# Optimization experiments

Hardware: AMD Instinct MI355X
Metric: run time of the kernel (lower is better)

## Reference

```python
import jax, jax.numpy as jnp
import numpy as np

N_EMBD = 1024
HEAD_SIZE = 64
B, T = 8, 2048


def setup_inputs() -> dict:
    key = jax.random.key(0)
    kx, kq, kk, kv = jax.random.split(key, 4)
    s = 1.0 / np.sqrt(N_EMBD)  # ~ torch Linear init scale
    return {
        "x": jax.random.normal(kx, (B, T, N_EMBD), dtype=jnp.float32),
        "Wq": jax.random.normal(kq, (N_EMBD, HEAD_SIZE), dtype=jnp.float32) * s,
        "Wk": jax.random.normal(kk, (N_EMBD, HEAD_SIZE), dtype=jnp.float32) * s,
        "Wv": jax.random.normal(kv, (N_EMBD, HEAD_SIZE), dtype=jnp.float32) * s,
    }


def reference(x, Wq, Wk, Wv):
    # x: [B,T,C]; single-head causal self-attention (dropout p=0.0 / eval)
    q = jnp.einsum("btc,cd->btd", x, Wq)
    k = jnp.einsum("btc,cd->btd", x, Wk)
    v = jnp.einsum("btc,cd->btd", x, Wv)
    scale = 1.0 / np.sqrt(HEAD_SIZE).astype(np.float32)
    scores = jnp.einsum("bqd,bkd->bqk", q, k) * scale  # [B,T,T]
    Tq = x.shape[1]
    causal = jnp.tril(jnp.ones((Tq, Tq), dtype=bool))
    scores = jnp.where(causal[None, :, :], scores, -jnp.inf)
    attn = jax.nn.softmax(scores, axis=-1)
    out = jnp.einsum("bqk,bkd->bqd", attn, v)  # [B,T,head_size]
    return out
```

## Files before the change

### kernel.cpp

```cpp
#include <hip/hip_runtime.h>
#include <hip/hip_bf16.h>

#define BATCH 8
#define SEQ   2048
#define CDIM  1024
#define HDIM  64
#define NROWS (BATCH*SEQ)
#define NSPLIT 8

typedef __attribute__((ext_vector_type(8))) short bf16x8;
typedef __attribute__((ext_vector_type(4))) float f32x4;

#define QSCALE 0.18033688011112042f
#define SFIX 24.0f

__device__ inline ushort f2bf(float f) {
    union { float f; uint u; } x; x.f = f;
    uint r = (x.u + 0x7fffu + ((x.u >> 16) & 1u)) >> 16;
    return (ushort)r;
}

__global__ __launch_bounds__(256) void wpack_kernel(
    const float* __restrict__ Wq, const float* __restrict__ Wk,
    const float* __restrict__ Wv, ushort* __restrict__ wp2)
{
    const int g = blockIdx.x * 256 + threadIdx.x;
    const int l15  = g & 15;
    const int hi   = (g >> 4) & 3;
    const int c32  = (g >> 6) & 1;
    const int step = (g >> 7) & 15;
    const int f    = g >> 11;
    const int n = f * 16 + l15;
    const int which = n >> 6, nl = n & 63;
    const float* W = (which == 0) ? Wq : (which == 1) ? Wk : Wv;
    const float sc = (which == 0) ? QSCALE : 1.0f;
    const int c0 = step * 64 + c32 * 32 + hi * 8;

    ushort v[8];
    #pragma unroll
    for (int j = 0; j < 8; ++j)
        v[j] = f2bf(W[(size_t)(c0 + j) * HDIM + nl] * sc);
    uint4 pack;
    pack.x = (uint)v[0] | ((uint)v[1] << 16);
    pack.y = (uint)v[2] | ((uint)v[3] << 16);
    pack.z = (uint)v[4] | ((uint)v[5] << 16);
    pack.w = (uint)v[6] | ((uint)v[7] << 16);
    reinterpret_cast<uint4*>(wp2)[g] = pack;
}

__global__ __launch_bounds__(512, 4) void qkv_gemm(
    const float* __restrict__ x, const ushort* __restrict__ wp2,
    ushort* __restrict__ qb, ushort* __restrict__ kbuf, ushort* __restrict__ vt)
{
    __shared__ ushort xs[2][32 * 64];
    const int t = threadIdx.x;
    const int w = t >> 6, lane = t & 63;
    const int l15 = lane & 15, hi = lane >> 4;
    const int rowg = w & 1, colg = w >> 1;
    const int m0 = blockIdx.x * 32;

    f32x4 acc[3];
    #pragma unroll
    for (int i = 0; i < 3; ++i) acc[i] = (f32x4){0.f, 0.f, 0.f, 0.f};

    const int xrow = t >> 4, xc4 = t & 15;
    float4 xra, xrb;
    const ushort* wbase = wp2 + (size_t)lane * 8;

#define LOADX(S, KK)                                                           \
    xr##S = reinterpret_cast<const float4*>(x + (size_t)(m0 + xrow) * CDIM + (KK))[xc4];

#define WRITEX(S, BUF)                                                         \
    {                                                                          \
        ushort4 bx = make_ushort4(f2bf(xr##S.x), f2bf(xr##S.y), f2bf(xr##S.z), f2bf(xr##S.w)); \
        int xb = (xrow * 128 + xc4 * 8) ^ ((xrow & 7) << 4);                   \
        *reinterpret_cast<ushort4*>(reinterpret_cast<char*>(xs[BUF]) + xb) = bx; \
    }

#define MFMA_STEP(BUF, STEP)                                                   \
    {                                                                          \
        const int arow = rowg * 16 + l15;                                      \
        bf16x8 bf[6];                                                          \
        _Pragma("unroll")                                                      \
        for (int nf = 0; nf < 3; ++nf) {                                       \
            const int f = colg * 3 + nf;                                       \
            bf[nf * 2 + 0] = *reinterpret_cast<const bf16x8*>(wbase + (size_t)(f * 16 + (STEP)) * 1024);       \
            bf[nf * 2 + 1] = *reinterpret_cast<const bf16x8*>(wbase + (size_t)(f * 16 + (STEP)) * 1024 + 512); \
        }                                                                      \
        _Pragma("unroll")                                                      \
        for (int c32 = 0; c32 < 2; ++c32) {                                    \
            const int abyte = (arow * 128 + hi * 16 + c32 * 64) ^ ((arow & 7) << 4); \
            bf16x8 a = *reinterpret_cast<const bf16x8*>(reinterpret_cast<char*>(xs[BUF]) + abyte); \
            _Pragma("unroll")                                                  \
            for (int nf = 0; nf < 3; ++nf)                                     \
                acc[nf] = __builtin_amdgcn_mfma_f32_16x16x32_bf16(a, bf[nf * 2 + c32], acc[nf], 0, 0, 0); \
        }                                                                      \
    }

    LOADX(a, 0)
    LOADX(b, 64)
    WRITEX(a, 0)
    __syncthreads();

    for (int step = 0; step < 16; step += 2) {
        if (step + 2 < 16) { LOADX(a, (step + 2) * 64) }
        MFMA_STEP(0, step)
        WRITEX(b, 1)
        __syncthreads();
        if (step + 3 < 16) { LOADX(b, (step + 3) * 64) }
        MFMA_STEP(1, step + 1)
        if (step + 2 < 16) { WRITEX(a, 0) }
        __syncthreads();
    }
#undef LOADX
#undef WRITEX
#undef MFMA_STEP

    #pragma unroll
    for (int nf = 0; nf < 3; ++nf) {
        const int n = colg * 48 + nf * 16 + l15;
        #pragma unroll
        for (int r = 0; r < 4; ++r) {
            const int grow = m0 + rowg * 16 + hi * 4 + r;
            const ushort bv = f2bf(acc[nf][r]);
            if (n < 64) {
                qb[(size_t)grow * 64 + n] = bv;
            } else if (n < 128) {
                kbuf[(size_t)grow * 64 + (n - 64)] = bv;
            } else {
                const int b = grow >> 11, tt = grow & 2047;
                vt[(((size_t)b * 64 + (n - 128)) << 11) + tt] = bv;
            }
        }
    }
}

__global__ __launch_bounds__(256, 4) void attn_flash(
    const ushort* __restrict__ qb, const ushort* __restrict__ kbuf,
    const ushort* __restrict__ vt, ushort* __restrict__ Opart,
    float* __restrict__ lpart)
{
    __shared__ ushort kst[2][64 * 64];
    __shared__ ushort vst[2][64 * 64];
    __shared__ ushort P[4][1024];

    const int t = threadIdx.x;
    const int w = t >> 6, lane = t & 63;
    const int l15 = lane & 15, hi = lane >> 4;
    const int bid = blockIdx.x;
    const int pid = (bid & 7) * 128 + (bid >> 3);
    const int batch = pid >> 7;
    const int rem = pid & 127;
    const int pairIdx = rem >> 3;
    const int s = rem & 7;
    const int qtA = pairIdx, qtB = 31 - pairIdx;
    const int ntA = qtA + 1;

    const ushort* kB = kbuf + (size_t)batch * SEQ * 64;
    const ushort* vB = vt + (size_t)batch * 64 * SEQ;
    ushort* Osp = Opart + (size_t)s * NROWS * 64;
    float* lsp = lpart + (size_t)s * NROWS;
    char* pw = reinterpret_cast<char*>(P[w]);

    const int r0 = t >> 3, c8 = t & 7;
    const int r1 = r0 + 32;
    const int sb0 = (r0 * 128 + c8 * 16) ^ ((r0 & 7) << 4);
    const int sb1 = (r1 * 128 + c8 * 16) ^ ((r1 & 7) << 4);

    uint4 kr0, kr1, vr0, vr1;

#define STAGE_ISSUE(C)                                                        \
    {                                                                         \
        const int kt_ = ((C) >= ntA) ? ((C) - ntA) : (C);                     \
        const int j0_ = kt_ * 64;                                             \
        kr0 = *reinterpret_cast<const uint4*>(kB + (size_t)(j0_ + r0) * 64 + c8 * 8); \
        kr1 = *reinterpret_cast<const uint4*>(kB + (size_t)(j0_ + r1) * 64 + c8 * 8); \
        vr0 = *reinterpret_cast<const uint4*>(vB + (size_t)r0 * SEQ + j0_ + c8 * 8);  \
        vr1 = *reinterpret_cast<const uint4*>(vB + (size_t)r1 * SEQ + j0_ + c8 * 8);  \
    }

#define STAGE_WRITE(BUF)                                                      \
    {                                                                         \
        *reinterpret_cast<uint4*>(reinterpret_cast<char*>(kst[BUF]) + sb0) = kr0; \
        *reinterpret_cast<uint4*>(reinterpret_cast<char*>(kst[BUF]) + sb1) = kr1; \
        *reinterpret_cast<uint4*>(reinterpret_cast<char*>(vst[BUF]) + sb0) = vr0; \
        *reinterpret_cast<uint4*>(reinterpret_cast<char*>(vst[BUF]) + sb1) = vr1; \
    }

#define LOADQ(QT)                                                             \
    {                                                                         \
        const ushort* qp_ = qb + (size_t)(batch * SEQ + (QT) * 64 + w * 16 + l15) * 64 + hi * 8; \
        aq0 = *reinterpret_cast<const bf16x8*>(qp_);                          \
        aq1 = *reinterpret_cast<const bf16x8*>(qp_ + 32);                     \
    }

#define DUMP(QT)                                                              \
    {                                                                         \
        _Pragma("unroll")                                                     \
        for (int dt = 0; dt < 4; ++dt)                                        \
            _Pragma("unroll")                                                 \
            for (int r = 0; r < 4; ++r)                                       \
                Osp[(size_t)(batch * SEQ + (QT) * 64 + w * 16 + hi * 4 + r) * 64 + dt * 16 + l15] = f2bf(O[dt][r]); \
        _Pragma("unroll")                                                     \
        for (int r = 0; r < 4; ++r) {                                         \
            float s_ = lsum[r];                                               \
            s_ += __shfl_xor(s_, 1, 64);                                      \
            s_ += __shfl_xor(s_, 2, 64);                                      \
            s_ += __shfl_xor(s_, 4, 64);                                      \
            s_ += __shfl_xor(s_, 8, 64);                                      \
            if (l15 == 0)                                                     \
                lsp[batch * SEQ + (QT) * 64 + w * 16 + hi * 4 + r] = s_;      \
        }                                                                     \
    }

#define RESET_STATE()                                                         \
    {                                                                         \
        _Pragma("unroll")                                                     \
        for (int i = 0; i < 4; ++i) {                                         \
            O[i] = (f32x4){0.f, 0.f, 0.f, 0.f};                               \
            lsum[i] = 0.f;                                                    \
        }                                                                     \
    }

    bf16x8 aq0, aq1;
    LOADQ(qtA)
    f32x4 O[4];
    float lsum[4];
    RESET_STATE()

    STAGE_ISSUE(s)
    STAGE_WRITE(0)
    __syncthreads();

    int curB = 0, cur = 0;
    for (int c = s; c < 33; c += 8) {
        if (c + 8 < 33) { STAGE_ISSUE(c + 8) }
        if (c >= ntA && !curB) {
            DUMP(qtA)
            RESET_STATE()
            LOADQ(qtB)
            curB = 1;
        }
        const int qt = curB ? qtB : qtA;
        const int kt = curB ? (c - ntA) : c;
        const int j0 = kt * 64;
        const int qrow0 = qt * 64 + w * 16;
        const bool diag = curB ? (c == 32) : (c == ntA - 1);

        const char* kc = reinterpret_cast<const char*>(kst[cur]);
        const char* vc = reinterpret_cast<const char*>(vst[cur]);

        f32x4 S[4];
        #pragma unroll
        for (int kb = 0; kb < 4; ++kb) {
            const int key = kb * 16 + l15;
            const int sw = (key & 7) << 4;
            bf16x8 b0 = *reinterpret_cast<const bf16x8*>(kc + ((key * 128 + hi * 16) ^ sw));
            bf16x8 b1 = *reinterpret_cast<const bf16x8*>(kc + ((key * 128 + hi * 16 + 64) ^ sw));
            f32x4 z = (f32x4){0.f, 0.f, 0.f, 0.f};
            z = __builtin_amdgcn_mfma_f32_16x16x32_bf16(aq0, b0, z, 0, 0, 0);
            z = __builtin_amdgcn_mfma_f32_16x16x32_bf16(aq1, b1, z, 0, 0, 0);
            S[kb] = z;
        }
        if (diag) {
            #pragma unroll
            for (int kb = 0; kb < 4; ++kb) {
                const int key = j0 + kb * 16 + l15;
                #pragma unroll
                for (int r = 0; r < 4; ++r) {
                    const int qr = qrow0 + hi * 4 + r;
                    if (key > qr) S[kb][r] = -1e30f;
                }
            }
        }
        #pragma unroll
        for (int kb = 0; kb < 4; ++kb)
            #pragma unroll
            for (int r = 0; r < 4; ++r)
                S[kb][r] = exp2f(S[kb][r] - SFIX);
        #pragma unroll
        for (int r = 0; r < 4; ++r)
            lsum[r] += (S[0][r] + S[1][r]) + (S[2][r] + S[3][r]);

        #pragma unroll
        for (int kb = 0; kb < 4; ++kb) {
            #pragma unroll
            for (int r = 0; r < 4; ++r) {
                const int prow = hi * 4 + r;
                const int pcol = kb * 16 + l15;
                const int byte = (prow * 128 + pcol * 2) ^ ((prow & 7) << 4);
                *reinterpret_cast<ushort*>(pw + byte) = f2bf(S[kb][r]);
            }
        }
        asm volatile("" ::: "memory");
        const int pb0 = (l15 * 128 + hi * 16) ^ ((l15 & 7) << 4);
        const int pb1 = (l15 * 128 + hi * 16 + 64) ^ ((l15 & 7) << 4);
        bf16x8 pa0 = *reinterpret_cast<const bf16x8*>(pw + pb0);
        bf16x8 pa1 = *reinterpret_cast<const bf16x8*>(pw + pb1);
        #pragma unroll
        for (int dt = 0; dt < 4; ++dt) {
            const int d = dt * 16 + l15;
            const int sw = (d & 7) << 4;
            bf16x8 v0 = *reinterpret_cast<const bf16x8*>(vc + ((d * 128 + hi * 16) ^ sw));
            bf16x8 v1 = *reinterpret_cast<const bf16x8*>(vc + ((d * 128 + hi * 16 + 64) ^ sw));
            O[dt] = __builtin_amdgcn_mfma_f32_16x16x32_bf16(pa0, v0, O[dt], 0, 0, 0);
            O[dt] = __builtin_amdgcn_mfma_f32_16x16x32_bf16(pa1, v1, O[dt], 0, 0, 0);
        }
        if (c + 8 < 33) { STAGE_WRITE(cur ^ 1) }
        __syncthreads();
        cur ^= 1;
    }

    DUMP(qtB)
#undef STAGE_ISSUE
#undef STAGE_WRITE
#undef LOADQ
#undef DUMP
#undef RESET_STATE
}

__global__ __launch_bounds__(256) void merge_kernel(
    const ushort* __restrict__ Opart, const float* __restrict__ lpart,
    float* __restrict__ out)
{
    const int idx = blockIdx.x * 256 + threadIdx.x;
    const int row = idx >> 3;
    float acc[8] = {0.f, 0.f, 0.f, 0.f, 0.f, 0.f, 0.f, 0.f};
    float lv = 0.f;
    #pragma unroll
    for (int s = 0; s < NSPLIT; ++s) {
        uint4 v = reinterpret_cast<const uint4*>(Opart + (size_t)s * NROWS * 64)[idx];
        const uint u0 = v.x, u1 = v.y, u2 = v.z, u3 = v.w;
        acc[0] += __uint_as_float((u0 & 0xffffu) << 16);
        acc[1] += __uint_as_float(u0 & 0xffff0000u);
        acc[2] += __uint_as_float((u1 & 0xffffu) << 16);
        acc[3] += __uint_as_float(u1 & 0xffff0000u);
        acc[4] += __uint_as_float((u2 & 0xffffu) << 16);
        acc[5] += __uint_as_float(u2 & 0xffff0000u);
        acc[6] += __uint_as_float((u3 & 0xffffu) << 16);
        acc[7] += __uint_as_float(u3 & 0xffff0000u);
        lv += lpart[s * NROWS + row];
    }
    const float inv = 1.0f / lv;
    float4 o0 = make_float4(acc[0] * inv, acc[1] * inv, acc[2] * inv, acc[3] * inv);
    float4 o1 = make_float4(acc[4] * inv, acc[5] * inv, acc[6] * inv, acc[7] * inv);
    reinterpret_cast<float4*>(out)[idx * 2]     = o0;
    reinterpret_cast<float4*>(out)[idx * 2 + 1] = o1;
}

extern "C" void kernel_launch(void* const* d_in, const int* in_sizes, int n_in,
                              void* d_out, int out_size, void* d_ws, size_t ws_size,
                              hipStream_t stream) {
    const float* x  = (const float*)d_in[0];
    const float* Wq = (const float*)d_in[1];
    const float* Wk = (const float*)d_in[2];
    const float* Wv = (const float*)d_in[3];
    float* out = (float*)d_out;

    ushort* qb   = (ushort*)d_ws;
    ushort* kbuf = qb + (size_t)NROWS * 64;
    ushort* vt   = kbuf + (size_t)NROWS * 64;
    ushort* wp2  = vt + (size_t)NROWS * 64;
    float* lpart = (float*)(wp2 + 192 * 1024);
    ushort* Opart = (ushort*)(lpart + (size_t)NSPLIT * NROWS);

    wpack_kernel<<<96, 256, 0, stream>>>(Wq, Wk, Wv, wp2);
    qkv_gemm<<<NROWS / 32, 512, 0, stream>>>(x, wp2, qb, kbuf, vt);
    attn_flash<<<1024, 256, 0, stream>>>(qb, kbuf, vt, Opart, lpart);
    merge_kernel<<<(NROWS * HDIM / 8) / 256, 256, 0, stream>>>(Opart, lpart, out);
}
```

Baseline: 53.40 us.

## Stage packed QKV weights into LDS with async direct global-to-LDS loads

The weight pack is changed to a swizzled per-step layout, and the QKV GEMM now copies each 64-wide K-step of the weights into a double-buffered LDS tile with global_load_lds. It then reads the B fragments from LDS instead of having every wave fetch them from global memory. This removes the duplicated global/L2 weight traffic across the row groups and lets the weight loads overlap with the MFMA work. In exchange it adds 48KB of LDS per block, which likely cuts the number of resident blocks per CU below the launch-bounds target. Correctness also relies on the barriers waiting for the async LDS loads to finish.

Result: no change. 52.44 us (-1.8%).

```diff
diff --git a/kernel.cpp b/kernel.cpp
--- a/kernel.cpp
+++ b/kernel.cpp
@@ -20,39 +20,45 @@
     return (ushort)r;
 }
 
+__device__ inline void gload_lds16(const void* gsrc, void* ldst) {
+    __builtin_amdgcn_global_load_lds(
+        (const __attribute__((address_space(1))) unsigned int*)gsrc,
+        (__attribute__((address_space(3))) unsigned int*)ldst,
+        16, 0, 0);
+}
+
 __global__ __launch_bounds__(256) void wpack_kernel(
     const float* __restrict__ Wq, const float* __restrict__ Wk,
-    const float* __restrict__ Wv, ushort* __restrict__ wp2)
+    const float* __restrict__ Wv, ushort* __restrict__ wp3)
 {
     const int g = blockIdx.x * 256 + threadIdx.x;
-    const int l15  = g & 15;
-    const int hi   = (g >> 4) & 3;
-    const int c32  = (g >> 6) & 1;
-    const int step = (g >> 7) & 15;
-    const int f    = g >> 11;
-    const int n = f * 16 + l15;
+    const int s = g / 1536;
+    const int i = g % 1536;
+    const int n = i >> 3;
+    const int b0 = ((i & 7) * 16) ^ ((n & 7) << 4);
+    const int c0 = s * 64 + (b0 >> 1);
     const int which = n >> 6, nl = n & 63;
     const float* W = (which == 0) ? Wq : (which == 1) ? Wk : Wv;
     const float sc = (which == 0) ? QSCALE : 1.0f;
-    const int c0 = step * 64 + c32 * 32 + hi * 8;
 
     ushort v[8];
     #pragma unroll
-    for (int j = 0; j < 8; ++j)
-        v[j] = f2bf(W[(size_t)(c0 + j) * HDIM + nl] * sc);
+    for (int k = 0; k < 8; ++k)
+        v[k] = f2bf(W[(size_t)(c0 + k) * HDIM + nl] * sc);
     uint4 pack;
     pack.x = (uint)v[0] | ((uint)v[1] << 16);
     pack.y = (uint)v[2] | ((uint)v[3] << 16);
     pack.z = (uint)v[4] | ((uint)v[5] << 16);
     pack.w = (uint)v[6] | ((uint)v[7] << 16);
-    reinterpret_cast<uint4*>(wp2)[g] = pack;
+    reinterpret_cast<uint4*>(wp3)[g] = pack;
 }
 
 __global__ __launch_bounds__(512, 4) void qkv_gemm(
-    const float* __restrict__ x, const ushort* __restrict__ wp2,
+    const float* __restrict__ x, const ushort* __restrict__ wp3,
     ushort* __restrict__ qb, ushort* __restrict__ kbuf, ushort* __restrict__ vt)
 {
     __shared__ ushort xs[2][32 * 64];
+    __shared__ ushort ws[2][192 * 64];
     const int t = threadIdx.x;
     const int w = t >> 6, lane = t & 63;
     const int l15 = lane & 15, hi = lane >> 4;
@@ -65,7 +71,16 @@
 
     const int xrow = t >> 4, xc4 = t & 15;
     float4 xra, xrb;
-    const ushort* wbase = wp2 + (size_t)lane * 8;
+
+#define GLOADW(STEP, BUF)                                                      \
+    {                                                                          \
+        _Pragma("unroll")                                                      \
+        for (int j = 0; j < 3; ++j) {                                          \
+            const int chunk = j * 512 + w * 64;                                \
+            gload_lds16(wp3 + ((size_t)(STEP) * 1536 + chunk + lane) * 8,      \
+                        reinterpret_cast<char*>(ws[BUF]) + chunk * 16);        \
+        }                                                                      \
+    }
 
 #define LOADX(S, KK)                                                           \
     xr##S = reinterpret_cast<const float4*>(x + (size_t)(m0 + xrow) * CDIM + (KK))[xc4];
@@ -77,26 +92,25 @@
         *reinterpret_cast<ushort4*>(reinterpret_cast<char*>(xs[BUF]) + xb) = bx; \
     }
 
-#define MFMA_STEP(BUF, STEP)                                                   \
+#define MFMA_STEP(BUF)                                                         \
     {                                                                          \
         const int arow = rowg * 16 + l15;                                      \
-        bf16x8 bf[6];                                                          \
-        _Pragma("unroll")                                                      \
-        for (int nf = 0; nf < 3; ++nf) {                                       \
-            const int f = colg * 3 + nf;                                       \
-            bf[nf * 2 + 0] = *reinterpret_cast<const bf16x8*>(wbase + (size_t)(f * 16 + (STEP)) * 1024);       \
-            bf[nf * 2 + 1] = *reinterpret_cast<const bf16x8*>(wbase + (size_t)(f * 16 + (STEP)) * 1024 + 512); \
-        }                                                                      \
         _Pragma("unroll")                                                      \
         for (int c32 = 0; c32 < 2; ++c32) {                                    \
             const int abyte = (arow * 128 + hi * 16 + c32 * 64) ^ ((arow & 7) << 4); \
             bf16x8 a = *reinterpret_cast<const bf16x8*>(reinterpret_cast<char*>(xs[BUF]) + abyte); \
             _Pragma("unroll")                                                  \
-            for (int nf = 0; nf < 3; ++nf)                                     \
-                acc[nf] = __builtin_amdgcn_mfma_f32_16x16x32_bf16(a, bf[nf * 2 + c32], acc[nf], 0, 0, 0); \
+            for (int nf = 0; nf < 3; ++nf) {                                   \
+                const int n = colg * 48 + nf * 16 + l15;                       \
+                const int bbyte = (n * 128 + hi * 16 + c32 * 64) ^ ((n & 7) << 4); \
+                bf16x8 b = *reinterpret_cast<const bf16x8*>(reinterpret_cast<char*>(ws[BUF]) + bbyte); \
+                acc[nf] = __builtin_amdgcn_mfma_f32_16x16x32_bf16(a, b, acc[nf], 0, 0, 0); \
+            }                                                                  \
         }                                                                      \
     }
 
+    GLOADW(0, 0)
+    GLOADW(1, 1)
     LOADX(a, 0)
     LOADX(b, 64)
     WRITEX(a, 0)
@@ -104,14 +118,17 @@
 
     for (int step = 0; step < 16; step += 2) {
         if (step + 2 < 16) { LOADX(a, (step + 2) * 64) }
-        MFMA_STEP(0, step)
+        MFMA_STEP(0)
         WRITEX(b, 1)
         __syncthreads();
+        if (step + 2 < 16) { GLOADW(step + 2, 0) }
         if (step + 3 < 16) { LOADX(b, (step + 3) * 64) }
-        MFMA_STEP(1, step + 1)
+        MFMA_STEP(1)
         if (step + 2 < 16) { WRITEX(a, 0) }
         __syncthreads();
-    }
+        if (step + 3 < 16) { GLOADW(step + 3, 1) }
+    }
+#undef GLOADW
 #undef LOADX
 #undef WRITEX
 #undef MFMA_STEP
@@ -360,12 +377,12 @@
     ushort* qb   = (ushort*)d_ws;
     ushort* kbuf = qb + (size_t)NROWS * 64;
     ushort* vt   = kbuf + (size_t)NROWS * 64;
-    ushort* wp2  = vt + (size_t)NROWS * 64;
-    float* lpart = (float*)(wp2 + 192 * 1024);
+    ushort* wp3  = vt + (size_t)NROWS * 64;
+    float* lpart = (float*)(wp3 + 192 * 1024);
     ushort* Opart = (ushort*)(lpart + (size_t)NSPLIT * NROWS);
 
-    wpack_kernel<<<96, 256, 0, stream>>>(Wq, Wk, Wv, wp2);
-    qkv_gemm<<<NROWS / 32, 512, 0, stream>>>(x, wp2, qb, kbuf, vt);
+    wpack_kernel<<<96, 256, 0, stream>>>(Wq, Wk, Wv, wp3);
+    qkv_gemm<<<NROWS / 32, 512, 0, stream>>>(x, wp3, qb, kbuf, vt);
     attn_flash<<<1024, 256, 0, stream>>>(qb, kbuf, vt, Opart, lpart);
     merge_kernel<<<(NROWS * HDIM / 8) / 256, 256, 0, stream>>>(Opart, lpart, out);
 }
```
